# Kernel optimization log

Hardware: AMD Instinct MI355X
Metric: run time of the kernel (lower is better)

The kernel has to match this reference:

```python
import jax, jax.numpy as jnp
import numpy as np

B, S, F, E, R, O = 4, 2048, 2048, 16, 16, 2048
TEMPERATURE = 1.0


def setup_inputs() -> dict:
    key = jax.random.key(0)
    k1, k2, k3, k4 = jax.random.split(key, 4)
    x = jax.random.normal(k1, (B, S, F), dtype=jnp.float32)
    prototypes = jax.random.normal(k2, (E, F), dtype=jnp.float32)
    # prototypes are top right-singular vectors -> unit norm rows
    prototypes = prototypes / jnp.linalg.norm(prototypes, axis=1, keepdims=True)
    A_stack = jax.random.normal(k3, (E, R, F), dtype=jnp.float32) * 0.02
    B_stack = jax.random.normal(k4, (E, O, R), dtype=jnp.float32) * 0.02
    scaling = jnp.float32(2.0)
    return {"x": x, "prototypes": prototypes, "A_stack": A_stack,
            "B_stack": B_stack, "scaling": scaling, "top_k": 4}


def reference(x, prototypes, A_stack, B_stack, scaling, top_k):
    lead = x.shape[:-1]
    f_in = x.shape[-1]
    tok = x.reshape(-1, f_in)                       # (t, F)
    t = tok.shape[0]

    # Arrow routing: abs cosine-like similarity to per-expert prototypes
    sim = jnp.abs(tok @ prototypes.T)               # (t, E)
    top_v, idx = jax.lax.top_k(sim, top_k)          # (t, k)
    full_score = jnp.full(sim.shape, -jnp.inf, dtype=sim.dtype)
    full_score = full_score.at[jnp.arange(t)[:, None], idx].set(top_v)
    coeff = jax.nn.softmax(full_score / TEMPERATURE, axis=1)  # (t, E), zeros off top-k

    # Per-expert LoRA: z = tok @ A_e^T  (dense over all experts, as in source)
    z = jnp.einsum('tf,erf->ter', tok, A_stack)     # (t, E, r)
    # Combine coeff into the low-rank space before the B projection to avoid
    # materializing the (t, E, out) tensor; math identical to
    # einsum('te, teo -> to', coeff, einsum('ter,eor->teo', z, B_stack)).
    delta = jnp.einsum('te,ter,eor->to', coeff, z, B_stack)  # (t, O)

    delta = scaling * delta                          # dropout = identity (eval)
    return delta.reshape(lead + (delta.shape[-1],))
```

## Files before the change

### kernel.cpp

```cpp
#include <hip/hip_runtime.h>
#include <hip/hip_bf16.h>
#include <stdint.h>

#define T_TOKENS 8192
#define F_DIM    2048
#define E_EXP    16
#define R_RANK   16
#define O_DIM    2048
#define KDIM     (E_EXP * R_RANK)

typedef short v8s __attribute__((ext_vector_type(8)));
typedef float v4f __attribute__((ext_vector_type(4)));

#define AS1 __attribute__((address_space(1)))
#define AS3 __attribute__((address_space(3)))

__device__ __forceinline__ uint16_t f2bf(float f) {
  uint32_t u = __builtin_bit_cast(uint32_t, f);
  u += 0x7fffu + ((u >> 16) & 1u);
  return (uint16_t)(u >> 16);
}

__device__ __forceinline__ void g2lds16(const void* g, void* l) {
  __builtin_amdgcn_global_load_lds((const AS1 void*)g, (AS3 void*)l, 16, 0, 0);
}

__global__ __launch_bounds__(256) void prep_weights(
    const float* __restrict__ A, const float* __restrict__ Bst,
    uint16_t* __restrict__ Ab, uint16_t* __restrict__ Bb) {
  int idx = blockIdx.x * 256 + threadIdx.x;
  if (idx < KDIM * F_DIM) {
    Ab[idx] = f2bf(A[idx]);
  }
  if (idx < O_DIM * KDIM) {
    int k = idx & (KDIM - 1);
    int o = idx >> 8;
    int e = k >> 4, r = k & 15;
    Bb[idx] = f2bf(Bst[((size_t)e * O_DIM + o) * R_RANK + r]);
  }
}

__global__ __launch_bounds__(256) void route_stream(
    const float* __restrict__ x, const float* __restrict__ P,
    uint16_t* __restrict__ xb, float4* __restrict__ partials4) {
  __shared__ float ps[16 * 256];
  const int tid = threadIdx.x;
  const int c   = blockIdx.x;
  const int by  = blockIdx.y;
  const int f0  = c * 256;

  #pragma unroll
  for (int p = 0; p < 4; ++p) {
    const int G = p * 256 + tid;
    g2lds16(&P[(size_t)(G >> 6) * F_DIM + f0 + (G & 63) * 4],
            (char*)ps + (p * 256 + (tid >> 6) * 64) * 16);
  }
  __syncthreads();

  const int sub = tid & 7;
  const int tg  = tid >> 3;
  const int row = by * 32 + tg;
  const float* xr = x  + (size_t)row * F_DIM + f0;
  uint16_t*    xw = xb + (size_t)row * F_DIM + f0;

  float a[16];
  #pragma unroll
  for (int e = 0; e < 16; ++e) a[e] = 0.f;

  float4 v[8];
  #pragma unroll
  for (int k = 0; k < 8; ++k)
    v[k] = *(const float4*)&xr[sub * 4 + k * 32];

  #pragma unroll
  for (int k = 0; k < 8; ++k) {
    uint2 pk;
    pk.x = (uint32_t)f2bf(v[k].x) | ((uint32_t)f2bf(v[k].y) << 16);
    pk.y = (uint32_t)f2bf(v[k].z) | ((uint32_t)f2bf(v[k].w) << 16);
    *(uint2*)&xw[sub * 4 + k * 32] = pk;
  }

  #pragma unroll
  for (int k = 0; k < 8; ++k) {
    const int col = sub * 4 + k * 32;
    #pragma unroll
    for (int e = 0; e < 16; ++e) {
      float4 pv = *(float4*)&ps[e * 256 + col];
      a[e] += v[k].x * pv.x; a[e] += v[k].y * pv.y;
      a[e] += v[k].z * pv.z; a[e] += v[k].w * pv.w;
    }
  }

  #pragma unroll
  for (int m = 1; m <= 4; m <<= 1) {
    #pragma unroll
    for (int e = 0; e < 16; ++e)
      a[e] += __shfl_xor(a[e], m, 64);
  }

  if (sub < 4) {
    partials4[((size_t)c * 4 + sub) * T_TOKENS + row] =
        make_float4(a[sub * 4], a[sub * 4 + 1], a[sub * 4 + 2], a[sub * 4 + 3]);
  }
}

__global__ __launch_bounds__(256) void gemm_xa(
    const uint16_t* __restrict__ xb, const uint16_t* __restrict__ Ab,
    const float4* __restrict__ partials4, const float* __restrict__ scaling,
    const int* __restrict__ topk, uint16_t* __restrict__ wb) {
  __shared__ uint16_t S[16384];
  __shared__ float coeffL[64 * 17];
  uint16_t* Xh[2] = { S,         S + 4096  };
  uint16_t* Ah[2] = { S + 8192,  S + 12288 };
  const int tid  = threadIdx.x;
  const int b    = blockIdx.x;
  const int m_idx = (b & 7) + ((b >> 5) << 3);
  const int n_idx = (b >> 3) & 3;
  const int m0 = m_idx * 64, n0 = n_idx * 64;
  const int lane = tid & 63;
  const int wid  = tid >> 6;
  const int wm   = (wid >> 1) * 32;
  const int wn   = (wid & 1) * 32;
  const int quad = lane >> 4;
  const int cl   = lane & 15;

  if (tid < 64) {
    const int t = m0 + tid;
    double s[16];
    #pragma unroll
    for (int e = 0; e < 16; ++e) s[e] = 0.0;
    for (int c = 0; c < 8; ++c) {
      #pragma unroll
      for (int e4 = 0; e4 < 4; ++e4) {
        float4 p = partials4[((size_t)c * 4 + e4) * T_TOKENS + t];
        s[e4 * 4]     += (double)p.x;
        s[e4 * 4 + 1] += (double)p.y;
        s[e4 * 4 + 2] += (double)p.z;
        s[e4 * 4 + 3] += (double)p.w;
      }
    }
    double v[16];
    #pragma unroll
    for (int e = 0; e < 16; ++e) v[e] = fabs(s[e]);
    int k = topk[0];
    if (k > 16) k = 16;
    if (k < 1)  k = 1;
    unsigned mask = 0;
    double mx = 0.0;
    float ssum = 0.f;
    for (int i = 0; i < k; ++i) {
      double bv = -1.0; int bj = 0;
      #pragma unroll
      for (int j = 0; j < 16; ++j) {
        bool ok = !((mask >> j) & 1u) && (v[j] > bv);
        bv = ok ? v[j] : bv;
        bj = ok ? j  : bj;
      }
      mask |= 1u << bj;
      if (i == 0) mx = bv;
      ssum += expf((float)(bv - mx));
    }
    const float sc = scaling[0];
    #pragma unroll
    for (int j = 0; j < 16; ++j)
      coeffL[tid * 17 + j] = ((mask >> j) & 1u)
          ? expf((float)(v[j] - mx)) / ssum * sc : 0.f;
  }

  const int G0 = wid * 64 + lane;
  const int G1 = G0 + 256;
  const int r0 = G0 >> 3, g0 = (G0 & 7) ^ (r0 & 7);
  const int r1 = G1 >> 3, g1 = (G1 & 7) ^ (r1 & 7);
  const uint16_t* xs0 = xb + (size_t)(m0 + r0) * F_DIM + g0 * 8;
  const uint16_t* xs1 = xb + (size_t)(m0 + r1) * F_DIM + g1 * 8;
  const uint16_t* as0 = Ab + (size_t)(n0 + r0) * F_DIM + g0 * 8;
  const uint16_t* as1 = Ab + (size_t)(n0 + r1) * F_DIM + g1 * 8;
  const int d0 = wid * 512;
  const int d1 = wid * 512 + 2048;

  const int ma0 = wm + cl, ma1 = wm + 16 + cl;
  const int nb0 = wn + cl, nb1 = wn + 16 + cl;

  v4f acc[2][2];
  #pragma unroll
  for (int i = 0; i < 2; i++)
    #pragma unroll
    for (int j = 0; j < 2; j++) acc[i][j] = (v4f){0.f, 0.f, 0.f, 0.f};

  for (int k0 = 0; k0 < F_DIM; k0 += 128) {
    __syncthreads();
    g2lds16(xs0 + k0,      Xh[0] + d0);
    g2lds16(xs1 + k0,      Xh[0] + d1);
    g2lds16(as0 + k0,      Ah[0] + d0);
    g2lds16(as1 + k0,      Ah[0] + d1);
    g2lds16(xs0 + k0 + 64, Xh[1] + d0);
    g2lds16(xs1 + k0 + 64, Xh[1] + d1);
    g2lds16(as0 + k0 + 64, Ah[1] + d0);
    g2lds16(as1 + k0 + 64, Ah[1] + d1);
    __syncthreads();
    #pragma unroll
    for (int h = 0; h < 2; ++h) {
      #pragma unroll
      for (int ks = 0; ks < 2; ++ks) {
        const int gk = ks * 4 + quad;
        v8s fa0 = *(v8s*)&Xh[h][(ma0 * 8 + (gk ^ (ma0 & 7))) * 8];
        v8s fa1 = *(v8s*)&Xh[h][(ma1 * 8 + (gk ^ (ma1 & 7))) * 8];
        v8s fb0 = *(v8s*)&Ah[h][(nb0 * 8 + (gk ^ (nb0 & 7))) * 8];
        v8s fb1 = *(v8s*)&Ah[h][(nb1 * 8 + (gk ^ (nb1 & 7))) * 8];
        acc[0][0] = __builtin_amdgcn_mfma_f32_16x16x32_bf16(fa0, fb0, acc[0][0], 0, 0, 0);
        acc[0][1] = __builtin_amdgcn_mfma_f32_16x16x32_bf16(fa0, fb1, acc[0][1], 0, 0, 0);
        acc[1][0] = __builtin_amdgcn_mfma_f32_16x16x32_bf16(fa1, fb0, acc[1][0], 0, 0, 0);
        acc[1][1] = __builtin_amdgcn_mfma_f32_16x16x32_bf16(fa1, fb1, acc[1][1], 0, 0, 0);
      }
    }
  }

  __syncthreads();
  uint16_t* tile = S;
  #pragma unroll
  for (int mi = 0; mi < 2; mi++)
    #pragma unroll
    for (int ni = 0; ni < 2; ni++) {
      const int nl = wn + ni * 16 + cl;
      const int eidx = (n0 + nl) >> 4;
      #pragma unroll
      for (int reg = 0; reg < 4; reg++) {
        const int tl = wm + mi * 16 + quad * 4 + reg;
        float wv = acc[mi][ni][reg] * coeffL[tl * 17 + eidx];
        tile[tl * 72 + nl] = f2bf(wv);
      }
    }
  __syncthreads();
  #pragma unroll
  for (int p = 0; p < 2; ++p) {
    const int row  = p * 32 + (tid >> 3);
    const int colg = (tid & 7) * 8;
    uint4 val = *(uint4*)&tile[row * 72 + colg];
    *(uint4*)&wb[(size_t)(m0 + row) * KDIM + n0 + colg] = val;
  }
}

__global__ __launch_bounds__(256) void gemm_wb(
    const uint16_t* __restrict__ wbuf, const uint16_t* __restrict__ Bb,
    float* __restrict__ out) {
  __shared__ uint16_t S[20480];
  uint16_t* Ws = S;
  uint16_t* Bs = S + 4096;
  const int tid  = threadIdx.x;
  const int b    = blockIdx.x;
  const int m_idx = (b & 7) + ((b >> 6) << 3);
  const int n_idx = (b >> 3) & 7;
  const int m0 = m_idx * 64;
  const int n0 = n_idx * 256;
  const int lane = tid & 63;
  const int wid  = tid >> 6;
  const int wm   = (wid >> 1) * 32;
  const int wn   = (wid & 1) * 128;
  const int quad = lane >> 4;
  const int cl   = lane & 15;

  const int GW0 = wid * 64 + lane;
  const int GW1 = GW0 + 256;
  const int wr0 = GW0 >> 3, wg0 = (GW0 & 7) ^ (wr0 & 7);
  const int wr1 = GW1 >> 3, wg1 = (GW1 & 7) ^ (wr1 & 7);
  const uint16_t* wsrc0 = wbuf + (size_t)(m0 + wr0) * KDIM + wg0 * 8;
  const uint16_t* wsrc1 = wbuf + (size_t)(m0 + wr1) * KDIM + wg1 * 8;

  const uint16_t* bsrc[8];
  #pragma unroll
  for (int p = 0; p < 8; ++p) {
    const int G = p * 256 + wid * 64 + lane;
    const int r = G >> 3, g = (G & 7) ^ (r & 7);
    bsrc[p] = Bb + (size_t)(n0 + r) * KDIM + g * 8;
  }

  v4f acc[2][8];
  #pragma unroll
  for (int i = 0; i < 2; i++)
    #pragma unroll
    for (int j = 0; j < 8; j++) acc[i][j] = (v4f){0.f, 0.f, 0.f, 0.f};

  const int ma0 = wm + cl, ma1 = wm + 16 + cl;

  #pragma unroll
  for (int k0 = 0; k0 < KDIM; k0 += 64) {
    __syncthreads();
    g2lds16(wsrc0 + k0, Ws + wid * 512);
    g2lds16(wsrc1 + k0, Ws + wid * 512 + 2048);
    #pragma unroll
    for (int p = 0; p < 8; ++p)
      g2lds16(bsrc[p] + k0, Bs + (p * 256 + wid * 64) * 8);
    __syncthreads();
    #pragma unroll
    for (int ks = 0; ks < 2; ++ks) {
      const int gk = ks * 4 + quad;
      v8s fa0 = *(v8s*)&Ws[(ma0 * 8 + (gk ^ (ma0 & 7))) * 8];
      v8s fa1 = *(v8s*)&Ws[(ma1 * 8 + (gk ^ (ma1 & 7))) * 8];
      v8s fb[8];
      #pragma unroll
      for (int j = 0; j < 8; ++j) {
        const int nb = wn + j * 16 + cl;
        fb[j] = *(v8s*)&Bs[(nb * 8 + (gk ^ (nb & 7))) * 8];
      }
      #pragma unroll
      for (int j = 0; j < 8; ++j) {
        acc[0][j] = __builtin_amdgcn_mfma_f32_16x16x32_bf16(fa0, fb[j], acc[0][j], 0, 0, 0);
        acc[1][j] = __builtin_amdgcn_mfma_f32_16x16x32_bf16(fa1, fb[j], acc[1][j], 0, 0, 0);
      }
    }
  }

  float* ft = (float*)S;
  #pragma unroll
  for (int h = 0; h < 2; ++h) {
    __syncthreads();
    if ((wid >> 1) == h) {
      #pragma unroll
      for (int mi = 0; mi < 2; mi++)
        #pragma unroll
        for (int j = 0; j < 8; j++) {
          const int col = wn + j * 16 + cl;
          #pragma unroll
          for (int reg = 0; reg < 4; reg++) {
            const int rl = mi * 16 + quad * 4 + reg;
            ft[rl * 260 + col] = acc[mi][j][reg];
          }
        }
    }
    __syncthreads();
    #pragma unroll
    for (int p = 0; p < 8; ++p) {
      const int f4  = p * 256 + tid;
      const int row = f4 >> 6;
      const int c4  = f4 & 63;
      float4 v = *(float4*)&ft[row * 260 + c4 * 4];
      *(float4*)&out[(size_t)(m0 + h * 32 + row) * O_DIM + n0 + c4 * 4] = v;
    }
  }
}

extern "C" void kernel_launch(void* const* d_in, const int* in_sizes, int n_in,
                              void* d_out, int out_size, void* d_ws, size_t ws_size,
                              hipStream_t stream) {
  (void)in_sizes; (void)n_in; (void)out_size; (void)ws_size;
  const float* x       = (const float*)d_in[0];
  const float* P       = (const float*)d_in[1];
  const float* A       = (const float*)d_in[2];
  const float* Bst     = (const float*)d_in[3];
  const float* scaling = (const float*)d_in[4];
  const int*   topk    = (const int*)d_in[5];
  float* out = (float*)d_out;

  char* ws = (char*)d_ws;
  uint16_t* xb     = (uint16_t*)(ws);
  uint16_t* Ab     = (uint16_t*)(ws + 33554432);
  uint16_t* Bb     = (uint16_t*)(ws + 34603008);
  uint16_t* wbuf   = (uint16_t*)(ws + 35651584);
  float4*   parts  = (float4*)  (ws + 39845888);

  hipLaunchKernelGGL(prep_weights, dim3(2048), dim3(256), 0, stream, A, Bst, Ab, Bb);
  hipLaunchKernelGGL(route_stream, dim3(8, 256), dim3(256), 0, stream, x, P, xb, parts);
  hipLaunchKernelGGL(gemm_xa, dim3(512), dim3(256), 0, stream,
                     xb, Ab, parts, scaling, topk, wbuf);
  hipLaunchKernelGGL(gemm_wb, dim3(1024), dim3(256), 0, stream, wbuf, Bb, out);
}
```

Measured before the change: 165.4 us.

## Restructure x·A GEMM to full-N tiles with direct-global A fragments and double buffering

```diff
diff --git a/kernel.cpp b/kernel.cpp
--- a/kernel.cpp
+++ b/kernel.cpp
@@ -104,27 +104,22 @@
   }
 }
 
-__global__ __launch_bounds__(256) void gemm_xa(
+__global__ __launch_bounds__(512) void gemm_xa(
     const uint16_t* __restrict__ xb, const uint16_t* __restrict__ Ab,
     const float4* __restrict__ partials4, const float* __restrict__ scaling,
     const int* __restrict__ topk, uint16_t* __restrict__ wb) {
-  __shared__ uint16_t S[16384];
-  __shared__ float coeffL[64 * 17];
-  uint16_t* Xh[2] = { S,         S + 4096  };
-  uint16_t* Ah[2] = { S + 8192,  S + 12288 };
+  __shared__ uint16_t S[8448];
+  __shared__ float coeffL[32 * 17];
+  uint16_t* X0 = S;
+  uint16_t* X1 = S + 4096;
   const int tid  = threadIdx.x;
-  const int b    = blockIdx.x;
-  const int m_idx = (b & 7) + ((b >> 5) << 3);
-  const int n_idx = (b >> 3) & 3;
-  const int m0 = m_idx * 64, n0 = n_idx * 64;
+  const int m0   = blockIdx.x * 32;
   const int lane = tid & 63;
   const int wid  = tid >> 6;
-  const int wm   = (wid >> 1) * 32;
-  const int wn   = (wid & 1) * 32;
   const int quad = lane >> 4;
   const int cl   = lane & 15;
 
-  if (tid < 64) {
+  if (tid < 32) {
     const int t = m0 + tid;
     double s[16];
     #pragma unroll
@@ -167,19 +162,20 @@
           ? expf((float)(v[j] - mx)) / ssum * sc : 0.f;
   }
 
-  const int G0 = wid * 64 + lane;
-  const int G1 = G0 + 256;
-  const int r0 = G0 >> 3, g0 = (G0 & 7) ^ (r0 & 7);
-  const int r1 = G1 >> 3, g1 = (G1 & 7) ^ (r1 & 7);
-  const uint16_t* xs0 = xb + (size_t)(m0 + r0) * F_DIM + g0 * 8;
-  const uint16_t* xs1 = xb + (size_t)(m0 + r1) * F_DIM + g1 * 8;
-  const uint16_t* as0 = Ab + (size_t)(n0 + r0) * F_DIM + g0 * 8;
-  const uint16_t* as1 = Ab + (size_t)(n0 + r1) * F_DIM + g1 * 8;
-  const int d0 = wid * 512;
-  const int d1 = wid * 512 + 2048;
-
-  const int ma0 = wm + cl, ma1 = wm + 16 + cl;
-  const int nb0 = wn + cl, nb1 = wn + 16 + cl;
+  const int sr   = tid >> 4;
+  const int slot = tid & 15;
+  const int sg   = (slot & 8) | ((slot & 7) ^ (sr & 7));
+  const uint16_t* xsrc = xb + (size_t)(m0 + sr) * F_DIM + sg * 8;
+  uint16_t* const ldst0 = X0 + tid * 8;
+  uint16_t* const ldst1 = X1 + tid * 8;
+
+  const uint16_t* Apt[2];
+  #pragma unroll
+  for (int j = 0; j < 2; ++j)
+    Apt[j] = Ab + (size_t)(wid * 32 + j * 16 + cl) * F_DIM + quad * 8;
+
+  const char* faB = (char*)S + cl * 256;
+  const int   clx = cl & 7;
 
   v4f acc[2][2];
   #pragma unroll
@@ -187,57 +183,60 @@
     #pragma unroll
     for (int j = 0; j < 2; j++) acc[i][j] = (v4f){0.f, 0.f, 0.f, 0.f};
 
-  for (int k0 = 0; k0 < F_DIM; k0 += 128) {
-    __syncthreads();
-    g2lds16(xs0 + k0,      Xh[0] + d0);
-    g2lds16(xs1 + k0,      Xh[0] + d1);
-    g2lds16(as0 + k0,      Ah[0] + d0);
-    g2lds16(as1 + k0,      Ah[0] + d1);
-    g2lds16(xs0 + k0 + 64, Xh[1] + d0);
-    g2lds16(xs1 + k0 + 64, Xh[1] + d1);
-    g2lds16(as0 + k0 + 64, Ah[1] + d0);
-    g2lds16(as1 + k0 + 64, Ah[1] + d1);
-    __syncthreads();
-    #pragma unroll
-    for (int h = 0; h < 2; ++h) {
-      #pragma unroll
-      for (int ks = 0; ks < 2; ++ks) {
-        const int gk = ks * 4 + quad;
-        v8s fa0 = *(v8s*)&Xh[h][(ma0 * 8 + (gk ^ (ma0 & 7))) * 8];
-        v8s fa1 = *(v8s*)&Xh[h][(ma1 * 8 + (gk ^ (ma1 & 7))) * 8];
-        v8s fb0 = *(v8s*)&Ah[h][(nb0 * 8 + (gk ^ (nb0 & 7))) * 8];
-        v8s fb1 = *(v8s*)&Ah[h][(nb1 * 8 + (gk ^ (nb1 & 7))) * 8];
-        acc[0][0] = __builtin_amdgcn_mfma_f32_16x16x32_bf16(fa0, fb0, acc[0][0], 0, 0, 0);
-        acc[0][1] = __builtin_amdgcn_mfma_f32_16x16x32_bf16(fa0, fb1, acc[0][1], 0, 0, 0);
-        acc[1][0] = __builtin_amdgcn_mfma_f32_16x16x32_bf16(fa1, fb0, acc[1][0], 0, 0, 0);
-        acc[1][1] = __builtin_amdgcn_mfma_f32_16x16x32_bf16(fa1, fb1, acc[1][1], 0, 0, 0);
-      }
-    }
+#define STAGE_X(dst_, kk) g2lds16(xsrc + (kk), dst_)
+
+#define COMP_X(base_, kelem_) do {                                                        \
+    _Pragma("unroll")                                                                     \
+    for (int s = 0; s < 4; ++s) {                                                         \
+      const int gk = s * 4 + quad;                                                        \
+      const int sl = (gk & 8) | ((gk & 7) ^ clx);                                         \
+      v8s fa0 = *(const v8s*)((base_) + sl * 16);                                         \
+      v8s fa1 = *(const v8s*)((base_) + 4096 + sl * 16);                                  \
+      v8s fb0 = *(const v8s*)(Apt[0] + (kelem_) + s * 32);                                \
+      v8s fb1 = *(const v8s*)(Apt[1] + (kelem_) + s * 32);                                \
+      acc[0][0] = __builtin_amdgcn_mfma_f32_16x16x32_bf16(fa0, fb0, acc[0][0], 0, 0, 0);  \
+      acc[0][1] = __builtin_amdgcn_mfma_f32_16x16x32_bf16(fa0, fb1, acc[0][1], 0, 0, 0);  \
+      acc[1][0] = __builtin_amdgcn_mfma_f32_16x16x32_bf16(fa1, fb0, acc[1][0], 0, 0, 0);  \
+      acc[1][1] = __builtin_amdgcn_mfma_f32_16x16x32_bf16(fa1, fb1, acc[1][1], 0, 0, 0);  \
+    }                                                                                     \
+  } while (0)
+
+
+  STAGE_X(ldst0, 0);
+  for (int k0 = 0; k0 < F_DIM; k0 += 256) {
+    __syncthreads();
+    STAGE_X(ldst1, k0 + 128);
+    COMP_X(faB, k0);
+    __syncthreads();
+    if (k0 + 256 < F_DIM) STAGE_X(ldst0, k0 + 256);
+    COMP_X(faB + 8192, k0 + 128);
   }
 
   __syncthreads();
   uint16_t* tile = S;
   #pragma unroll
-  for (int mi = 0; mi < 2; mi++)
-    #pragma unroll
-    for (int ni = 0; ni < 2; ni++) {
-      const int nl = wn + ni * 16 + cl;
-      const int eidx = (n0 + nl) >> 4;
-      #pragma unroll
-      for (int reg = 0; reg < 4; reg++) {
-        const int tl = wm + mi * 16 + quad * 4 + reg;
-        float wv = acc[mi][ni][reg] * coeffL[tl * 17 + eidx];
-        tile[tl * 72 + nl] = f2bf(wv);
+  for (int mi = 0; mi < 2; ++mi)
+    #pragma unroll
+    for (int ni = 0; ni < 2; ++ni) {
+      const int col = wid * 32 + ni * 16 + cl;
+      const int e   = wid * 2 + ni;
+      #pragma unroll
+      for (int reg = 0; reg < 4; ++reg) {
+        const int tl = mi * 16 + quad * 4 + reg;
+        tile[tl * 264 + col] = f2bf(acc[mi][ni][reg] * coeffL[tl * 17 + e]);
       }
     }
   __syncthreads();
   #pragma unroll
   for (int p = 0; p < 2; ++p) {
-    const int row  = p * 32 + (tid >> 3);
-    const int colg = (tid & 7) * 8;
-    uint4 val = *(uint4*)&tile[row * 72 + colg];
-    *(uint4*)&wb[(size_t)(m0 + row) * KDIM + n0 + colg] = val;
-  }
+    const int f4  = p * 512 + tid;
+    const int row = f4 >> 5;
+    const int c16 = f4 & 31;
+    *(uint4*)&wb[(size_t)(m0 + row) * KDIM + c16 * 8] =
+        *(uint4*)&tile[row * 264 + c16 * 8];
+  }
+#undef STAGE_X
+#undef COMP_X
 }
 
 __global__ __launch_bounds__(256) void gemm_wb(
@@ -360,7 +359,7 @@
 
   hipLaunchKernelGGL(prep_weights, dim3(2048), dim3(256), 0, stream, A, Bst, Ab, Bb);
   hipLaunchKernelGGL(route_stream, dim3(8, 256), dim3(256), 0, stream, x, P, xb, parts);
-  hipLaunchKernelGGL(gemm_xa, dim3(512), dim3(256), 0, stream,
+  hipLaunchKernelGGL(gemm_xa, dim3(256), dim3(512), 0, stream,
                      xb, Ab, parts, scaling, topk, wbuf);
   hipLaunchKernelGGL(gemm_wb, dim3(1024), dim3(256), 0, stream, wbuf, Bb, out);
 }
```

After: 183.9 us. 1.11x slower.
